# Performance work log

Measured on AMD Instinct MI355X. Metric: run time of the kernel, lower is better.

The kernel has to match this reference:

```python
import jax, jax.numpy as jnp
import numpy as np

B, L, C = 32, 8192, 64
LEVELS = 3  # detail kernels 3,5,9 with pads 1,2,4


def _conv1d(x, w, b, pad):
    # x: [B, C, L], w: [O, I, K] (torch Conv1d layout), b: [O]
    y = jax.lax.conv_general_dilated(
        x, w, window_strides=(1,), padding=[(pad, pad)],
        dimension_numbers=('NCH', 'OIH', 'NCH'))
    return y + b[None, :, None]


def _block(xc, w1, b1, w2, b2, pad):
    # Conv1d(k) -> ReLU -> Conv1d(k=1)
    h = jax.nn.relu(_conv1d(xc, w1, b1, pad))
    return _conv1d(h, w2, b2, 0)


def setup_inputs() -> dict:
    key = jax.random.key(0)
    ks = jax.random.split(key, 20)
    s = 0.05  # keep activations stable
    inp = {
        'x': jax.random.normal(ks[0], (B, L, C), jnp.float32),
        'rec_weights': jnp.ones((LEVELS + 1,), jnp.float32) / (LEVELS + 1),
        'trend_w1': jax.random.normal(ks[1], (C, C, 3), jnp.float32) * s,
        'trend_b1': jnp.zeros((C,), jnp.float32),
        'trend_w2': jax.random.normal(ks[2], (C, C, 1), jnp.float32) * s,
        'trend_b2': jnp.zeros((C,), jnp.float32),
    }
    kernels = [3, 5, 9]
    for i, k in enumerate(kernels, start=1):
        inp[f'd{i}_w1'] = jax.random.normal(ks[2 + 2 * i], (C, C, k), jnp.float32) * s
        inp[f'd{i}_b1'] = jnp.zeros((C,), jnp.float32)
        inp[f'd{i}_w2'] = jax.random.normal(ks[3 + 2 * i], (C, C, 1), jnp.float32) * s
        inp[f'd{i}_b2'] = jnp.zeros((C,), jnp.float32)
    return inp


def reference(x, rec_weights,
              trend_w1, trend_b1, trend_w2, trend_b2,
              d1_w1, d1_b1, d1_w2, d1_b2,
              d2_w1, d2_b1, d2_w2, d2_b2,
              d3_w1, d3_b1, d3_w2, d3_b2):
    # component_fusion forward: x [B, L, C] -> [B, L, C]
    xc = jnp.transpose(x, (0, 2, 1))  # [B, C, L]
    trend = _block(xc, trend_w1, trend_b1, trend_w2, trend_b2, 1)
    d1 = _block(xc, d1_w1, d1_b1, d1_w2, d1_b2, 1)   # k=3, pad=1
    d2 = _block(xc, d2_w1, d2_b1, d2_w2, d2_b2, 2)   # k=5, pad=2
    d3 = _block(xc, d3_w1, d3_b1, d3_w2, d3_b2, 4)   # k=9, pad=4
    w = jax.nn.softmax(rec_weights)
    fused = w[0] * trend + w[1] * d1 + w[2] * d2 + w[3] * d3
    return jnp.transpose(fused, (0, 2, 1))
```

## Files before the change

### kernel.cpp

```cpp
#include <hip/hip_runtime.h>


constexpr int Bn = 32, Ln = 8192;
constexpr int NT = 256;
constexpr int HALO = 4;
constexpr int XROWS = NT + 2 * HALO;
constexpr int RS = 72;
constexpr int NSLICE = 24;

constexpr int BRS[NSLICE] = {0,0,0,0, 1,1,1,1, 2,2,2,2,2,2, 3,3,3,3,3,3,3,3,3,3};
constexpr int DKS[NSLICE] = {0,1,2,-1, 0,1,2,-1, 0,1,2,3,4,-1, 0,1,2,3,4,5,6,7,8,-1};
constexpr int PPB[4] = {1, 1, 2, 4};

using bf16x8 = __attribute__((ext_vector_type(8))) __bf16;
using f32x4  = __attribute__((ext_vector_type(4))) float;
using u16x8  = __attribute__((ext_vector_type(8))) unsigned short;
using u16x4  = __attribute__((ext_vector_type(4))) unsigned short;
using s16x4  = __attribute__((ext_vector_type(4))) short;

struct Ptrs {
    const float* x;
    const float* rw;
    const float* w1[4];
    const float* b1[4];
    const float* w2[4];
    const float* b2[4];
};

__device__ __forceinline__ unsigned short f2bf(float f) {
    __bf16 h = (__bf16)f;
    return __builtin_bit_cast(unsigned short, h);
}

#if defined(__has_builtin)
#  if __has_builtin(__builtin_amdgcn_mfma_f32_16x16x16bf16_1k)
#    define HAVE_MFMA16 1
#  endif
#endif

__device__ __forceinline__ void mfma16(f32x4& c, u16x4 a, u16x4 b) {
#ifdef HAVE_MFMA16
    c = __builtin_amdgcn_mfma_f32_16x16x16bf16_1k(
            __builtin_bit_cast(s16x4, a), __builtin_bit_cast(s16x4, b), c, 0, 0, 0);
#else
    asm("v_mfma_f32_16x16x16_bf16 %0, %1, %2, %0" : "+v"(c) : "v"(a), "v"(b));
#endif
}

__device__ __forceinline__ void stage_slice(const unsigned short* __restrict__ frag,
                                            unsigned short* wbuf, int s, int tid) {
    const unsigned short* g = frag + (size_t)s * 4096 + tid * 8;
    unsigned short* l = wbuf + (s & 3) * 4096 + tid * 8;
    __builtin_amdgcn_global_load_lds(
        (const __attribute__((address_space(1))) unsigned int*)g,
        (__attribute__((address_space(3))) unsigned int*)l, 16, 0, 0);
    __builtin_amdgcn_global_load_lds(
        (const __attribute__((address_space(1))) unsigned int*)(g + 2048),
        (__attribute__((address_space(3))) unsigned int*)(l + 2048), 16, 0, 0);
}

__global__ void prep_kernel(Ptrs p, unsigned short* __restrict__ frag, float* __restrict__ hdr) {
    int tid = threadIdx.x;
    float v0 = p.rw[0], v1 = p.rw[1], v2 = p.rw[2], v3 = p.rw[3];
    float m = fmaxf(fmaxf(v0, v1), fmaxf(v2, v3));
    float e0 = expf(v0 - m), e1 = expf(v1 - m), e2 = expf(v2 - m), e3 = expf(v3 - m);
    float s = e0 + e1 + e2 + e3;
    float w[4] = {e0 / s, e1 / s, e2 / s, e3 / s};

    if (blockIdx.x == 0) {
        if (tid < 4) hdr[tid] = w[tid];
        if (tid < 64) {
            float fb = 0.f;
            #pragma unroll
            for (int i = 0; i < 4; i++) fb += w[i] * p.b2[i][tid];
            hdr[4 + tid] = fb;
        }
    }

    const int kk[4] = {3, 3, 5, 9};
    const int sbase[4] = {0, 4, 8, 14};

    for (int idx = blockIdx.x * blockDim.x + tid; idx < NSLICE * 4096; idx += gridDim.x * blockDim.x) {
        int sl = idx >> 12;
        int e = idx & 4095;
        int br = 3;
        #pragma unroll
        for (int i = 2; i >= 0; i--) if (sl < sbase[i + 1]) br = i;
        int local = sl - sbase[br];
        unsigned short val;
        if (local < kk[br]) {
            int blk = e >> 9;
            int ks = blk >> 2, mt = blk & 3;
            int sub = e & 511;
            int lane = sub >> 3, j = sub & 7;
            int co = mt * 16 + (lane & 15);
            int ci = ks * 32 + (lane >> 4) * 8 + j;
            val = f2bf(p.w1[br][(co * 64 + ci) * kk[br] + local]);
        } else {
            int c = e >> 9;
            int sub = e & 511;
            int lane = sub >> 3;
            int rest = sub & 7;
            int h = rest >> 2, j = rest & 3;
            int f = c * 2 + h;
            int kb = f >> 2, mt = f & 3;
            int co = mt * 16 + (lane & 15);
            int ci = kb * 16 + (lane >> 4) * 4 + j;
            val = f2bf(w[br] * p.w2[br][co * 64 + ci]);
        }
        frag[idx] = val;
    }
}

template <int S>
__device__ __forceinline__ void period(const unsigned short* __restrict__ frag,
                                       unsigned short* wbuf,
                                       const unsigned short* xs,
                                       const float* b1l,
                                       int tid, int lane, int wl0,
                                       f32x4 (&acc)[4][4], f32x4 (&fused)[4][4],
                                       bf16x8 (&cur)[8], bf16x8 (&nxt)[8]) {
    if constexpr (S <= 21) asm volatile("s_waitcnt vmcnt(2)" ::: "memory");
    else                   asm volatile("s_waitcnt vmcnt(0)" ::: "memory");
    __builtin_amdgcn_sched_barrier(0);
    __builtin_amdgcn_s_barrier();
    __builtin_amdgcn_sched_barrier(0);

    if constexpr (S + 1 < NSLICE) {
        const unsigned short* nb = wbuf + ((S + 1) & 3) * 4096 + lane * 8;
        #pragma unroll
        for (int c = 0; c < 8; c++)
            nxt[c] = __builtin_bit_cast(bf16x8, *(const u16x8*)(nb + c * 512));
    }
    if constexpr (S + 3 < NSLICE) stage_slice(frag, wbuf, S + 3, tid);

    constexpr int br = BRS[S];
    constexpr int dk = DKS[S];
    int col = lane & 15, kg = lane >> 4;

    if constexpr (dk >= 0) {
        if constexpr (dk == 0) {
            #pragma unroll
            for (int mt = 0; mt < 4; mt++)
                #pragma unroll
                for (int nt = 0; nt < 4; nt++)
                    acc[mt][nt] = f32x4{0.f, 0.f, 0.f, 0.f};
        }
        constexpr int PP = PPB[br];
        #pragma unroll
        for (int ks = 0; ks < 2; ks++) {
            bf16x8 bfr[4];
            #pragma unroll
            for (int nt = 0; nt < 4; nt++) {
                int row = wl0 + nt * 16 + col + (HALO - PP) + dk;
                bfr[nt] = __builtin_bit_cast(bf16x8, *(const u16x8*)&xs[row * RS + ks * 32 + kg * 8]);
            }
            __builtin_amdgcn_s_setprio(1);
            #pragma unroll
            for (int mt = 0; mt < 4; mt++)
                #pragma unroll
                for (int nt = 0; nt < 4; nt++)
                    acc[mt][nt] = __builtin_amdgcn_mfma_f32_16x16x32_bf16(cur[ks * 4 + mt], bfr[nt], acc[mt][nt], 0, 0, 0);
            __builtin_amdgcn_s_setprio(0);
        }
    } else {
        const float* bb = b1l + br * 64;
        f32x4 bv[4];
        #pragma unroll
        for (int mt = 0; mt < 4; mt++) bv[mt] = *(const f32x4*)&bb[mt * 16 + kg * 4];
        #pragma unroll
        for (int kb = 0; kb < 4; kb++) {
            u16x4 hb[4];
            #pragma unroll
            for (int nt = 0; nt < 4; nt++) {
                u16x4 h;
                #pragma unroll
                for (int r = 0; r < 4; r++) h[r] = f2bf(fmaxf(acc[kb][nt][r] + bv[kb][r], 0.f));
                hb[nt] = h;
            }
            __builtin_amdgcn_s_setprio(1);
            #pragma unroll
            for (int mt2 = 0; mt2 < 4; mt2++) {
                constexpr int dummy = 0; (void)dummy;
                int f = kb * 4 + mt2;
                u16x8 u = __builtin_bit_cast(u16x8, cur[f >> 1]);
                int h4 = (f & 1) * 4;
                u16x4 afr = {u[h4], u[h4 + 1], u[h4 + 2], u[h4 + 3]};
                #pragma unroll
                for (int nt = 0; nt < 4; nt++)
                    mfma16(fused[mt2][nt], afr, hb[nt]);
            }
            __builtin_amdgcn_s_setprio(0);
        }
    }
}

template <int S>
__device__ __forceinline__ void chain(const unsigned short* __restrict__ frag,
                                      unsigned short* wbuf, const unsigned short* xs,
                                      const float* b1l, int tid, int lane, int wl0,
                                      f32x4 (&acc)[4][4], f32x4 (&fused)[4][4],
                                      bf16x8 (&A)[8], bf16x8 (&B)[8]) {
    if constexpr (S & 1) period<S>(frag, wbuf, xs, b1l, tid, lane, wl0, acc, fused, B, A);
    else                 period<S>(frag, wbuf, xs, b1l, tid, lane, wl0, acc, fused, A, B);
    if constexpr (S + 1 < NSLICE)
        chain<S + 1>(frag, wbuf, xs, b1l, tid, lane, wl0, acc, fused, A, B);
}

__global__ __launch_bounds__(256, 2) void wavelet_main(Ptrs p,
                                                       const unsigned short* __restrict__ frag,
                                                       const float* __restrict__ hdr,
                                                       float* __restrict__ out) {
    __shared__ unsigned short xs[XROWS * RS];
    __shared__ unsigned short wbuf[4 * 4096];
    __shared__ float b1l[4 * 64];
    __shared__ float fbl[64];

    int tid = threadIdx.x;
    int b = blockIdx.x >> 5;
    int t0 = (blockIdx.x & 31) * NT;

    {
        int c0 = (tid & 7) * 8;
        int rbase = tid >> 3;
        #pragma unroll
        for (int it = 0; it < 9; it++) {
            int rr = it * 32 + rbase;
            if (rr < XROWS) {
                int l = t0 + rr - HALO;
                u16x8 v = {0, 0, 0, 0, 0, 0, 0, 0};
                if (l >= 0 && l < Ln) {
                    const float* src = &p.x[((size_t)b * Ln + l) * 64 + c0];
                    f32x4 a0 = *(const f32x4*)src;
                    f32x4 a1 = *(const f32x4*)(src + 4);
                    #pragma unroll
                    for (int r = 0; r < 4; r++) { v[r] = f2bf(a0[r]); v[4 + r] = f2bf(a1[r]); }
                }
                *(u16x8*)&xs[rr * RS + c0] = v;
            }
        }
    }
    b1l[tid] = p.b1[tid >> 6][tid & 63];
    if (tid < 64) fbl[tid] = hdr[4 + tid];
    __builtin_amdgcn_sched_barrier(0);

    stage_slice(frag, wbuf, 0, tid);
    stage_slice(frag, wbuf, 1, tid);
    stage_slice(frag, wbuf, 2, tid);

    asm volatile("s_waitcnt vmcnt(4) lgkmcnt(0)" ::: "memory");
    __builtin_amdgcn_sched_barrier(0);
    __builtin_amdgcn_s_barrier();
    __builtin_amdgcn_sched_barrier(0);

    int lane = tid & 63;
    int wl0 = (tid >> 6) * 64;
    int kg = lane >> 4;

    bf16x8 A[8], B[8];
    {
        const unsigned short* b0 = wbuf + lane * 8;
        #pragma unroll
        for (int c = 0; c < 8; c++)
            A[c] = __builtin_bit_cast(bf16x8, *(const u16x8*)(b0 + c * 512));
    }

    f32x4 acc[4][4];
    f32x4 fused[4][4];
    #pragma unroll
    for (int mt = 0; mt < 4; mt++)
        #pragma unroll
        for (int nt = 0; nt < 4; nt++)
            fused[mt][nt] = f32x4{0.f, 0.f, 0.f, 0.f};

    chain<0>(frag, wbuf, xs, b1l, tid, lane, wl0, acc, fused, A, B);

#ifndef HAVE_MFMA16
    asm volatile("s_nop 7\ns_nop 7");
#endif

    int col = lane & 15;
    f32x4 fb[4];
    #pragma unroll
    for (int mt = 0; mt < 4; mt++) fb[mt] = *(const f32x4*)&fbl[mt * 16 + kg * 4];
    #pragma unroll
    for (int nt = 0; nt < 4; nt++) {
        int l = t0 + wl0 + nt * 16 + col;
        #pragma unroll
        for (int mt = 0; mt < 4; mt++) {
            f32x4 v;
            #pragma unroll
            for (int r = 0; r < 4; r++) v[r] = fused[mt][nt][r] + fb[mt][r];
            *(f32x4*)&out[((size_t)b * Ln + l) * 64 + mt * 16 + kg * 4] = v;
        }
    }
}

extern "C" void kernel_launch(void* const* d_in, const int* in_sizes, int n_in,
                              void* d_out, int out_size, void* d_ws, size_t ws_size,
                              hipStream_t stream) {
    Ptrs p;
    p.x  = (const float*)d_in[0];
    p.rw = (const float*)d_in[1];
    for (int i = 0; i < 4; i++) {
        p.w1[i] = (const float*)d_in[2 + 4 * i];
        p.b1[i] = (const float*)d_in[3 + 4 * i];
        p.w2[i] = (const float*)d_in[4 + 4 * i];
        p.b2[i] = (const float*)d_in[5 + 4 * i];
    }
    float* hdr = (float*)d_ws;
    unsigned short* frag = (unsigned short*)((char*)d_ws + 512);

    hipLaunchKernelGGL(prep_kernel, dim3(96), dim3(256), 0, stream, p, frag, hdr);
    hipLaunchKernelGGL(wavelet_main, dim3(Bn * (Ln / NT)), dim3(256), 0, stream, p, frag, hdr,
                       (float*)d_out);
}
```

Baseline: 68.33 us.

## Load weight fragments directly from global memory instead of staging through LDS

Removes the 4-slot LDS ring buffer for weight slices, together with its async global-to-LDS staging and the per-slice barriers. Each wave now reads the next slice's weight fragments straight from global memory (cached in L2/L1) into registers one period ahead. This drops 32KB of LDS and 24 block-wide barriers per block, which could allow more occupancy and less synchronization. The cost is that global-load latency is now hidden only by one period of compute, and each of the four waves fetches the same data separately.

Result: faster. 61.75 us, median of 2 (-9.6%).

```diff
diff --git a/kernel.cpp b/kernel.cpp
--- a/kernel.cpp
+++ b/kernel.cpp
@@ -45,18 +45,6 @@
 #else
     asm("v_mfma_f32_16x16x16_bf16 %0, %1, %2, %0" : "+v"(c) : "v"(a), "v"(b));
 #endif
-}
-
-__device__ __forceinline__ void stage_slice(const unsigned short* __restrict__ frag,
-                                            unsigned short* wbuf, int s, int tid) {
-    const unsigned short* g = frag + (size_t)s * 4096 + tid * 8;
-    unsigned short* l = wbuf + (s & 3) * 4096 + tid * 8;
-    __builtin_amdgcn_global_load_lds(
-        (const __attribute__((address_space(1))) unsigned int*)g,
-        (__attribute__((address_space(3))) unsigned int*)l, 16, 0, 0);
-    __builtin_amdgcn_global_load_lds(
-        (const __attribute__((address_space(1))) unsigned int*)(g + 2048),
-        (__attribute__((address_space(3))) unsigned int*)(l + 2048), 16, 0, 0);
 }
 
 __global__ void prep_kernel(Ptrs p, unsigned short* __restrict__ frag, float* __restrict__ hdr) {
@@ -114,25 +102,17 @@
 
 template <int S>
 __device__ __forceinline__ void period(const unsigned short* __restrict__ frag,
-                                       unsigned short* wbuf,
                                        const unsigned short* xs,
                                        const float* b1l,
-                                       int tid, int lane, int wl0,
+                                       int lane, int wl0,
                                        f32x4 (&acc)[4][4], f32x4 (&fused)[4][4],
                                        bf16x8 (&cur)[8], bf16x8 (&nxt)[8]) {
-    if constexpr (S <= 21) asm volatile("s_waitcnt vmcnt(2)" ::: "memory");
-    else                   asm volatile("s_waitcnt vmcnt(0)" ::: "memory");
-    __builtin_amdgcn_sched_barrier(0);
-    __builtin_amdgcn_s_barrier();
-    __builtin_amdgcn_sched_barrier(0);
-
     if constexpr (S + 1 < NSLICE) {
-        const unsigned short* nb = wbuf + ((S + 1) & 3) * 4096 + lane * 8;
+        const unsigned short* nb = frag + (size_t)(S + 1) * 4096 + lane * 8;
         #pragma unroll
         for (int c = 0; c < 8; c++)
             nxt[c] = __builtin_bit_cast(bf16x8, *(const u16x8*)(nb + c * 512));
     }
-    if constexpr (S + 3 < NSLICE) stage_slice(frag, wbuf, S + 3, tid);
 
     constexpr int br = BRS[S];
     constexpr int dk = DKS[S];
@@ -181,7 +161,6 @@
             __builtin_amdgcn_s_setprio(1);
             #pragma unroll
             for (int mt2 = 0; mt2 < 4; mt2++) {
-                constexpr int dummy = 0; (void)dummy;
                 int f = kb * 4 + mt2;
                 u16x8 u = __builtin_bit_cast(u16x8, cur[f >> 1]);
                 int h4 = (f & 1) * 4;
@@ -197,14 +176,14 @@
 
 template <int S>
 __device__ __forceinline__ void chain(const unsigned short* __restrict__ frag,
-                                      unsigned short* wbuf, const unsigned short* xs,
-                                      const float* b1l, int tid, int lane, int wl0,
+                                      const unsigned short* xs,
+                                      const float* b1l, int lane, int wl0,
                                       f32x4 (&acc)[4][4], f32x4 (&fused)[4][4],
                                       bf16x8 (&A)[8], bf16x8 (&B)[8]) {
-    if constexpr (S & 1) period<S>(frag, wbuf, xs, b1l, tid, lane, wl0, acc, fused, B, A);
-    else                 period<S>(frag, wbuf, xs, b1l, tid, lane, wl0, acc, fused, A, B);
+    if constexpr (S & 1) period<S>(frag, xs, b1l, lane, wl0, acc, fused, B, A);
+    else                 period<S>(frag, xs, b1l, lane, wl0, acc, fused, A, B);
     if constexpr (S + 1 < NSLICE)
-        chain<S + 1>(frag, wbuf, xs, b1l, tid, lane, wl0, acc, fused, A, B);
+        chain<S + 1>(frag, xs, b1l, lane, wl0, acc, fused, A, B);
 }
 
 __global__ __launch_bounds__(256, 2) void wavelet_main(Ptrs p,
@@ -212,7 +191,6 @@
                                                        const float* __restrict__ hdr,
                                                        float* __restrict__ out) {
     __shared__ unsigned short xs[XROWS * RS];
-    __shared__ unsigned short wbuf[4 * 4096];
     __shared__ float b1l[4 * 64];
     __shared__ float fbl[64];
 
@@ -242,16 +220,6 @@
     }
     b1l[tid] = p.b1[tid >> 6][tid & 63];
     if (tid < 64) fbl[tid] = hdr[4 + tid];
-    __builtin_amdgcn_sched_barrier(0);
-
-    stage_slice(frag, wbuf, 0, tid);
-    stage_slice(frag, wbuf, 1, tid);
-    stage_slice(frag, wbuf, 2, tid);
-
-    asm volatile("s_waitcnt vmcnt(4) lgkmcnt(0)" ::: "memory");
-    __builtin_amdgcn_sched_barrier(0);
-    __builtin_amdgcn_s_barrier();
-    __builtin_amdgcn_sched_barrier(0);
 
     int lane = tid & 63;
     int wl0 = (tid >> 6) * 64;
@@ -259,7 +227,7 @@
 
     bf16x8 A[8], B[8];
     {
-        const unsigned short* b0 = wbuf + lane * 8;
+        const unsigned short* b0 = frag + lane * 8;
         #pragma unroll
         for (int c = 0; c < 8; c++)
             A[c] = __builtin_bit_cast(bf16x8, *(const u16x8*)(b0 + c * 512));
@@ -273,7 +241,9 @@
         for (int nt = 0; nt < 4; nt++)
             fused[mt][nt] = f32x4{0.f, 0.f, 0.f, 0.f};
 
-    chain<0>(frag, wbuf, xs, b1l, tid, lane, wl0, acc, fused, A, B);
+    __syncthreads();
+
+    chain<0>(frag, xs, b1l, lane, wl0, acc, fused, A, B);
 
 #ifndef HAVE_MFMA16
     asm volatile("s_nop 7\ns_nop 7");
```

## Process two weight slices per barrier with a five-slot LDS ring

Applied to the files above, without the earlier changes.

Restructures the weight pipeline so each barrier covers two slices instead of one, and enlarges the LDS ring from four to five slots. Two slices are staged per period, three to four slices ahead. The register double-buffer of next-slice weight fragments is removed; each slice now reads its fragments from LDS just before use. The aim is to halve barrier count and free VGPRs, at the cost of exposing LDS read latency before the MFMAs and using more shared memory per block, which may threaten two-blocks-per-CU occupancy.

New measurement: 66.08 us. 1.03x faster.

```diff
diff --git a/kernel.cpp b/kernel.cpp
--- a/kernel.cpp
+++ b/kernel.cpp
@@ -7,6 +7,7 @@
 constexpr int XROWS = NT + 2 * HALO;
 constexpr int RS = 72;
 constexpr int NSLICE = 24;
+constexpr int RING = 5;
 
 constexpr int BRS[NSLICE] = {0,0,0,0, 1,1,1,1, 2,2,2,2,2,2, 3,3,3,3,3,3,3,3,3,3};
 constexpr int DKS[NSLICE] = {0,1,2,-1, 0,1,2,-1, 0,1,2,3,4,-1, 0,1,2,3,4,5,6,7,8,-1};
@@ -47,10 +48,11 @@
 #endif
 }
 
+template <int S>
 __device__ __forceinline__ void stage_slice(const unsigned short* __restrict__ frag,
-                                            unsigned short* wbuf, int s, int tid) {
-    const unsigned short* g = frag + (size_t)s * 4096 + tid * 8;
-    unsigned short* l = wbuf + (s & 3) * 4096 + tid * 8;
+                                            unsigned short* wbuf, int tid) {
+    const unsigned short* g = frag + (size_t)S * 4096 + tid * 8;
+    unsigned short* l = wbuf + (S % RING) * 4096 + tid * 8;
     __builtin_amdgcn_global_load_lds(
         (const __attribute__((address_space(1))) unsigned int*)g,
         (__attribute__((address_space(3))) unsigned int*)l, 16, 0, 0);
@@ -113,30 +115,20 @@
 }
 
 template <int S>
-__device__ __forceinline__ void period(const unsigned short* __restrict__ frag,
-                                       unsigned short* wbuf,
-                                       const unsigned short* xs,
-                                       const float* b1l,
-                                       int tid, int lane, int wl0,
-                                       f32x4 (&acc)[4][4], f32x4 (&fused)[4][4],
-                                       bf16x8 (&cur)[8], bf16x8 (&nxt)[8]) {
-    if constexpr (S <= 21) asm volatile("s_waitcnt vmcnt(2)" ::: "memory");
-    else                   asm volatile("s_waitcnt vmcnt(0)" ::: "memory");
-    __builtin_amdgcn_sched_barrier(0);
-    __builtin_amdgcn_s_barrier();
-    __builtin_amdgcn_sched_barrier(0);
-
-    if constexpr (S + 1 < NSLICE) {
-        const unsigned short* nb = wbuf + ((S + 1) & 3) * 4096 + lane * 8;
-        #pragma unroll
-        for (int c = 0; c < 8; c++)
-            nxt[c] = __builtin_bit_cast(bf16x8, *(const u16x8*)(nb + c * 512));
-    }
-    if constexpr (S + 3 < NSLICE) stage_slice(frag, wbuf, S + 3, tid);
-
+__device__ __forceinline__ void slice_body(const unsigned short* wbuf,
+                                           const unsigned short* xs,
+                                           const float* b1l,
+                                           int lane, int wl0,
+                                           f32x4 (&acc)[4][4], f32x4 (&fused)[4][4]) {
     constexpr int br = BRS[S];
     constexpr int dk = DKS[S];
     int col = lane & 15, kg = lane >> 4;
+
+    const unsigned short* wb = wbuf + (S % RING) * 4096 + lane * 8;
+    bf16x8 wfr[8];
+    #pragma unroll
+    for (int c = 0; c < 8; c++)
+        wfr[c] = __builtin_bit_cast(bf16x8, *(const u16x8*)(wb + c * 512));
 
     if constexpr (dk >= 0) {
         if constexpr (dk == 0) {
@@ -160,7 +152,7 @@
             for (int mt = 0; mt < 4; mt++)
                 #pragma unroll
                 for (int nt = 0; nt < 4; nt++)
-                    acc[mt][nt] = __builtin_amdgcn_mfma_f32_16x16x32_bf16(cur[ks * 4 + mt], bfr[nt], acc[mt][nt], 0, 0, 0);
+                    acc[mt][nt] = __builtin_amdgcn_mfma_f32_16x16x32_bf16(wfr[ks * 4 + mt], bfr[nt], acc[mt][nt], 0, 0, 0);
             __builtin_amdgcn_s_setprio(0);
         }
     } else {
@@ -181,9 +173,8 @@
             __builtin_amdgcn_s_setprio(1);
             #pragma unroll
             for (int mt2 = 0; mt2 < 4; mt2++) {
-                constexpr int dummy = 0; (void)dummy;
                 int f = kb * 4 + mt2;
-                u16x8 u = __builtin_bit_cast(u16x8, cur[f >> 1]);
+                u16x8 u = __builtin_bit_cast(u16x8, wfr[f >> 1]);
                 int h4 = (f & 1) * 4;
                 u16x4 afr = {u[h4], u[h4 + 1], u[h4 + 2], u[h4 + 3]};
                 #pragma unroll
@@ -195,16 +186,34 @@
     }
 }
 
-template <int S>
+template <int P>
+__device__ __forceinline__ void period2(const unsigned short* __restrict__ frag,
+                                        unsigned short* wbuf,
+                                        const unsigned short* xs,
+                                        const float* b1l,
+                                        int tid, int lane, int wl0,
+                                        f32x4 (&acc)[4][4], f32x4 (&fused)[4][4]) {
+    if constexpr (P <= 10) asm volatile("s_waitcnt vmcnt(2)" ::: "memory");
+    else                   asm volatile("s_waitcnt vmcnt(0)" ::: "memory");
+    __builtin_amdgcn_sched_barrier(0);
+    __builtin_amdgcn_s_barrier();
+    __builtin_amdgcn_sched_barrier(0);
+
+    if constexpr (2 * P + 3 < NSLICE) stage_slice<(2 * P + 3) % NSLICE>(frag, wbuf, tid);
+    if constexpr (2 * P + 4 < NSLICE) stage_slice<(2 * P + 4) % NSLICE>(frag, wbuf, tid);
+
+    slice_body<2 * P>(wbuf, xs, b1l, lane, wl0, acc, fused);
+    slice_body<2 * P + 1>(wbuf, xs, b1l, lane, wl0, acc, fused);
+}
+
+template <int P>
 __device__ __forceinline__ void chain(const unsigned short* __restrict__ frag,
                                       unsigned short* wbuf, const unsigned short* xs,
                                       const float* b1l, int tid, int lane, int wl0,
-                                      f32x4 (&acc)[4][4], f32x4 (&fused)[4][4],
-                                      bf16x8 (&A)[8], bf16x8 (&B)[8]) {
-    if constexpr (S & 1) period<S>(frag, wbuf, xs, b1l, tid, lane, wl0, acc, fused, B, A);
-    else                 period<S>(frag, wbuf, xs, b1l, tid, lane, wl0, acc, fused, A, B);
-    if constexpr (S + 1 < NSLICE)
-        chain<S + 1>(frag, wbuf, xs, b1l, tid, lane, wl0, acc, fused, A, B);
+                                      f32x4 (&acc)[4][4], f32x4 (&fused)[4][4]) {
+    period2<P>(frag, wbuf, xs, b1l, tid, lane, wl0, acc, fused);
+    if constexpr (P + 1 < NSLICE / 2)
+        chain<P + 1>(frag, wbuf, xs, b1l, tid, lane, wl0, acc, fused);
 }
 
 __global__ __launch_bounds__(256, 2) void wavelet_main(Ptrs p,
@@ -212,7 +221,7 @@
                                                        const float* __restrict__ hdr,
                                                        float* __restrict__ out) {
     __shared__ unsigned short xs[XROWS * RS];
-    __shared__ unsigned short wbuf[4 * 4096];
+    __shared__ unsigned short wbuf[RING * 4096];
     __shared__ float b1l[4 * 64];
     __shared__ float fbl[64];
 
@@ -244,11 +253,11 @@
     if (tid < 64) fbl[tid] = hdr[4 + tid];
     __builtin_amdgcn_sched_barrier(0);
 
-    stage_slice(frag, wbuf, 0, tid);
-    stage_slice(frag, wbuf, 1, tid);
-    stage_slice(frag, wbuf, 2, tid);
-
-    asm volatile("s_waitcnt vmcnt(4) lgkmcnt(0)" ::: "memory");
+    stage_slice<0>(frag, wbuf, tid);
+    stage_slice<1>(frag, wbuf, tid);
+    stage_slice<2>(frag, wbuf, tid);
+
+    asm volatile("s_waitcnt lgkmcnt(0)" ::: "memory");
     __builtin_amdgcn_sched_barrier(0);
     __builtin_amdgcn_s_barrier();
     __builtin_amdgcn_sched_barrier(0);
@@ -256,14 +265,6 @@
     int lane = tid & 63;
     int wl0 = (tid >> 6) * 64;
     int kg = lane >> 4;
-
-    bf16x8 A[8], B[8];
-    {
-        const unsigned short* b0 = wbuf + lane * 8;
-        #pragma unroll
-        for (int c = 0; c < 8; c++)
-            A[c] = __builtin_bit_cast(bf16x8, *(const u16x8*)(b0 + c * 512));
-    }
 
     f32x4 acc[4][4];
     f32x4 fused[4][4];
@@ -273,7 +274,7 @@
         for (int nt = 0; nt < 4; nt++)
             fused[mt][nt] = f32x4{0.f, 0.f, 0.f, 0.f};
 
-    chain<0>(frag, wbuf, xs, b1l, tid, lane, wl0, acc, fused, A, B);
+    chain<0>(frag, wbuf, xs, b1l, tid, lane, wl0, acc, fused);
 
 #ifndef HAVE_MFMA16
     asm volatile("s_nop 7\ns_nop 7");
```

## Halve time tile per block, drop register double-buffer, raise occupancy to three blocks

Applied to the files above, without the earlier changes.

Each block now covers 128 time steps instead of 256, so each wave handles 32 columns and keeps half as many accumulators. Weight fragments are read from LDS at the start of each slice rather than prefetched into a second register set, and the next slice's async stage is issued after compute instead of before. Launch bounds ask for three blocks per CU to hide latency with more resident waves. In exchange, the grid doubles, each weight slice is staged from global memory twice as often per output, halo overhead per tile grows, and the LDS weight-fragment load now sits on the critical path of every slice.

Result: faster. 66.09 us (-3.3%).

```diff
diff --git a/kernel.cpp b/kernel.cpp
--- a/kernel.cpp
+++ b/kernel.cpp
@@ -2,11 +2,12 @@
 
 
 constexpr int Bn = 32, Ln = 8192;
-constexpr int NT = 256;
+constexpr int NT = 128;
 constexpr int HALO = 4;
 constexpr int XROWS = NT + 2 * HALO;
 constexpr int RS = 72;
 constexpr int NSLICE = 24;
+constexpr int RING = 4;
 
 constexpr int BRS[NSLICE] = {0,0,0,0, 1,1,1,1, 2,2,2,2,2,2, 3,3,3,3,3,3,3,3,3,3};
 constexpr int DKS[NSLICE] = {0,1,2,-1, 0,1,2,-1, 0,1,2,3,4,-1, 0,1,2,3,4,5,6,7,8,-1};
@@ -50,13 +51,23 @@
 __device__ __forceinline__ void stage_slice(const unsigned short* __restrict__ frag,
                                             unsigned short* wbuf, int s, int tid) {
     const unsigned short* g = frag + (size_t)s * 4096 + tid * 8;
-    unsigned short* l = wbuf + (s & 3) * 4096 + tid * 8;
+    unsigned short* l = wbuf + (s & (RING - 1)) * 4096 + tid * 8;
     __builtin_amdgcn_global_load_lds(
         (const __attribute__((address_space(1))) unsigned int*)g,
         (__attribute__((address_space(3))) unsigned int*)l, 16, 0, 0);
     __builtin_amdgcn_global_load_lds(
         (const __attribute__((address_space(1))) unsigned int*)(g + 2048),
         (__attribute__((address_space(3))) unsigned int*)(l + 2048), 16, 0, 0);
+}
+
+template <int N>
+__device__ __forceinline__ void wait_bar() {
+    if constexpr (N == 4)      asm volatile("s_waitcnt vmcnt(4)" ::: "memory");
+    else if constexpr (N == 2) asm volatile("s_waitcnt vmcnt(2)" ::: "memory");
+    else                       asm volatile("s_waitcnt vmcnt(0)" ::: "memory");
+    __builtin_amdgcn_sched_barrier(0);
+    __builtin_amdgcn_s_barrier();
+    __builtin_amdgcn_sched_barrier(0);
 }
 
 __global__ void prep_kernel(Ptrs p, unsigned short* __restrict__ frag, float* __restrict__ hdr) {
@@ -118,40 +129,35 @@
                                        const unsigned short* xs,
                                        const float* b1l,
                                        int tid, int lane, int wl0,
-                                       f32x4 (&acc)[4][4], f32x4 (&fused)[4][4],
-                                       bf16x8 (&cur)[8], bf16x8 (&nxt)[8]) {
-    if constexpr (S <= 21) asm volatile("s_waitcnt vmcnt(2)" ::: "memory");
-    else                   asm volatile("s_waitcnt vmcnt(0)" ::: "memory");
-    __builtin_amdgcn_sched_barrier(0);
-    __builtin_amdgcn_s_barrier();
-    __builtin_amdgcn_sched_barrier(0);
-
-    if constexpr (S + 1 < NSLICE) {
-        const unsigned short* nb = wbuf + ((S + 1) & 3) * 4096 + lane * 8;
-        #pragma unroll
-        for (int c = 0; c < 8; c++)
-            nxt[c] = __builtin_bit_cast(bf16x8, *(const u16x8*)(nb + c * 512));
-    }
-    if constexpr (S + 3 < NSLICE) stage_slice(frag, wbuf, S + 3, tid);
+                                       f32x4 (&acc)[4][2], f32x4 (&fused)[4][2]) {
+    if constexpr (S <= 21)      wait_bar<4>();
+    else if constexpr (S == 22) wait_bar<2>();
+    else                        wait_bar<0>();
 
     constexpr int br = BRS[S];
     constexpr int dk = DKS[S];
     int col = lane & 15, kg = lane >> 4;
 
+    const unsigned short* wb = wbuf + (S & (RING - 1)) * 4096 + lane * 8;
+    bf16x8 wfr[8];
+    #pragma unroll
+    for (int c = 0; c < 8; c++)
+        wfr[c] = __builtin_bit_cast(bf16x8, *(const u16x8*)(wb + c * 512));
+
     if constexpr (dk >= 0) {
         if constexpr (dk == 0) {
             #pragma unroll
             for (int mt = 0; mt < 4; mt++)
                 #pragma unroll
-                for (int nt = 0; nt < 4; nt++)
+                for (int nt = 0; nt < 2; nt++)
                     acc[mt][nt] = f32x4{0.f, 0.f, 0.f, 0.f};
         }
         constexpr int PP = PPB[br];
         #pragma unroll
         for (int ks = 0; ks < 2; ks++) {
-            bf16x8 bfr[4];
-            #pragma unroll
-            for (int nt = 0; nt < 4; nt++) {
+            bf16x8 bfr[2];
+            #pragma unroll
+            for (int nt = 0; nt < 2; nt++) {
                 int row = wl0 + nt * 16 + col + (HALO - PP) + dk;
                 bfr[nt] = __builtin_bit_cast(bf16x8, *(const u16x8*)&xs[row * RS + ks * 32 + kg * 8]);
             }
@@ -159,8 +165,8 @@
             #pragma unroll
             for (int mt = 0; mt < 4; mt++)
                 #pragma unroll
-                for (int nt = 0; nt < 4; nt++)
-                    acc[mt][nt] = __builtin_amdgcn_mfma_f32_16x16x32_bf16(cur[ks * 4 + mt], bfr[nt], acc[mt][nt], 0, 0, 0);
+                for (int nt = 0; nt < 2; nt++)
+                    acc[mt][nt] = __builtin_amdgcn_mfma_f32_16x16x32_bf16(wfr[ks * 4 + mt], bfr[nt], acc[mt][nt], 0, 0, 0);
             __builtin_amdgcn_s_setprio(0);
         }
     } else {
@@ -170,9 +176,9 @@
         for (int mt = 0; mt < 4; mt++) bv[mt] = *(const f32x4*)&bb[mt * 16 + kg * 4];
         #pragma unroll
         for (int kb = 0; kb < 4; kb++) {
-            u16x4 hb[4];
-            #pragma unroll
-            for (int nt = 0; nt < 4; nt++) {
+            u16x4 hb[2];
+            #pragma unroll
+            for (int nt = 0; nt < 2; nt++) {
                 u16x4 h;
                 #pragma unroll
                 for (int r = 0; r < 4; r++) h[r] = f2bf(fmaxf(acc[kb][nt][r] + bv[kb][r], 0.f));
@@ -181,50 +187,49 @@
             __builtin_amdgcn_s_setprio(1);
             #pragma unroll
             for (int mt2 = 0; mt2 < 4; mt2++) {
-                constexpr int dummy = 0; (void)dummy;
                 int f = kb * 4 + mt2;
-                u16x8 u = __builtin_bit_cast(u16x8, cur[f >> 1]);
+                u16x8 u = __builtin_bit_cast(u16x8, wfr[f >> 1]);
                 int h4 = (f & 1) * 4;
                 u16x4 afr = {u[h4], u[h4 + 1], u[h4 + 2], u[h4 + 3]};
                 #pragma unroll
-                for (int nt = 0; nt < 4; nt++)
+                for (int nt = 0; nt < 2; nt++)
                     mfma16(fused[mt2][nt], afr, hb[nt]);
             }
             __builtin_amdgcn_s_setprio(0);
         }
     }
+
+    if constexpr (S + 3 < NSLICE) stage_slice(frag, wbuf, S + 3, tid);
 }
 
 template <int S>
 __device__ __forceinline__ void chain(const unsigned short* __restrict__ frag,
                                       unsigned short* wbuf, const unsigned short* xs,
                                       const float* b1l, int tid, int lane, int wl0,
-                                      f32x4 (&acc)[4][4], f32x4 (&fused)[4][4],
-                                      bf16x8 (&A)[8], bf16x8 (&B)[8]) {
-    if constexpr (S & 1) period<S>(frag, wbuf, xs, b1l, tid, lane, wl0, acc, fused, B, A);
-    else                 period<S>(frag, wbuf, xs, b1l, tid, lane, wl0, acc, fused, A, B);
+                                      f32x4 (&acc)[4][2], f32x4 (&fused)[4][2]) {
+    period<S>(frag, wbuf, xs, b1l, tid, lane, wl0, acc, fused);
     if constexpr (S + 1 < NSLICE)
-        chain<S + 1>(frag, wbuf, xs, b1l, tid, lane, wl0, acc, fused, A, B);
-}
-
-__global__ __launch_bounds__(256, 2) void wavelet_main(Ptrs p,
+        chain<S + 1>(frag, wbuf, xs, b1l, tid, lane, wl0, acc, fused);
+}
+
+__global__ __launch_bounds__(256, 3) void wavelet_main(Ptrs p,
                                                        const unsigned short* __restrict__ frag,
                                                        const float* __restrict__ hdr,
                                                        float* __restrict__ out) {
     __shared__ unsigned short xs[XROWS * RS];
-    __shared__ unsigned short wbuf[4 * 4096];
+    __shared__ unsigned short wbuf[RING * 4096];
     __shared__ float b1l[4 * 64];
     __shared__ float fbl[64];
 
     int tid = threadIdx.x;
-    int b = blockIdx.x >> 5;
-    int t0 = (blockIdx.x & 31) * NT;
+    int b = blockIdx.x >> 6;
+    int t0 = (blockIdx.x & 63) * NT;
 
     {
         int c0 = (tid & 7) * 8;
         int rbase = tid >> 3;
         #pragma unroll
-        for (int it = 0; it < 9; it++) {
+        for (int it = 0; it < 5; it++) {
             int rr = it * 32 + rbase;
             if (rr < XROWS) {
                 int l = t0 + rr - HALO;
@@ -248,32 +253,24 @@
     stage_slice(frag, wbuf, 1, tid);
     stage_slice(frag, wbuf, 2, tid);
 
-    asm volatile("s_waitcnt vmcnt(4) lgkmcnt(0)" ::: "memory");
+    asm volatile("s_waitcnt lgkmcnt(0)" ::: "memory");
     __builtin_amdgcn_sched_barrier(0);
     __builtin_amdgcn_s_barrier();
     __builtin_amdgcn_sched_barrier(0);
 
     int lane = tid & 63;
-    int wl0 = (tid >> 6) * 64;
+    int wl0 = (tid >> 6) * 32;
     int kg = lane >> 4;
 
-    bf16x8 A[8], B[8];
-    {
-        const unsigned short* b0 = wbuf + lane * 8;
-        #pragma unroll
-        for (int c = 0; c < 8; c++)
-            A[c] = __builtin_bit_cast(bf16x8, *(const u16x8*)(b0 + c * 512));
-    }
-
-    f32x4 acc[4][4];
-    f32x4 fused[4][4];
+    f32x4 acc[4][2];
+    f32x4 fused[4][2];
     #pragma unroll
     for (int mt = 0; mt < 4; mt++)
         #pragma unroll
-        for (int nt = 0; nt < 4; nt++)
+        for (int nt = 0; nt < 2; nt++)
             fused[mt][nt] = f32x4{0.f, 0.f, 0.f, 0.f};
 
-    chain<0>(frag, wbuf, xs, b1l, tid, lane, wl0, acc, fused, A, B);
+    chain<0>(frag, wbuf, xs, b1l, tid, lane, wl0, acc, fused);
 
 #ifndef HAVE_MFMA16
     asm volatile("s_nop 7\ns_nop 7");
@@ -284,7 +281,7 @@
     #pragma unroll
     for (int mt = 0; mt < 4; mt++) fb[mt] = *(const f32x4*)&fbl[mt * 16 + kg * 4];
     #pragma unroll
-    for (int nt = 0; nt < 4; nt++) {
+    for (int nt = 0; nt < 2; nt++) {
         int l = t0 + wl0 + nt * 16 + col;
         #pragma unroll
         for (int mt = 0; mt < 4; mt++) {
```
